# Kernel optimization log

Hardware: AMD Instinct MI355X
Metric: run time of the kernel (lower is better)

Reference implementation:

```python
import jax, jax.numpy as jnp
import numpy as np

N, F, C, H, E, NC = 100000, 128, 64, 4, 1600000, 2
BN_EPS = 1e-5


def _bn(x, g, b):
    mu = x.mean(0)
    var = x.var(0)  # biased variance, as torch BN uses for normalization
    return (x - mu) / jnp.sqrt(var + BN_EPS) * g + b


def _gat(x, src, dst, W, a_src, a_dst, bias, heads, out_ch, concat, n):
    # x:[n,in] -> h:[n,heads,out_ch]
    h = (x @ W).reshape(n, heads, out_ch)
    e_src = (h * a_src[None]).sum(-1)  # [n,heads]
    e_dst = (h * a_dst[None]).sum(-1)
    logits = jax.nn.leaky_relu(e_src[src] + e_dst[dst], 0.2)  # [e,heads]
    m = jax.ops.segment_max(logits, dst, num_segments=n)
    m = jnp.where(jnp.isfinite(m), m, 0.0)
    ex = jnp.exp(logits - m[dst])
    denom = jax.ops.segment_sum(ex, dst, num_segments=n)
    alpha = ex / denom[dst]  # segment softmax over incoming edges
    out = jax.ops.segment_sum(alpha[:, :, None] * h[src], dst, num_segments=n)
    out = out.reshape(n, heads * out_ch) if concat else out.mean(axis=1)
    return out + bias


def _sage(x, src, dst, Wl, bl, Wr, n):
    agg = jax.ops.segment_sum(x[src], dst, num_segments=n)
    cnt = jax.ops.segment_sum(jnp.ones_like(src, dtype=x.dtype), dst, num_segments=n)
    agg = agg / jnp.maximum(cnt, 1.0)[:, None]  # mean aggregation
    return agg @ Wl + bl + x @ Wr


def setup_inputs() -> dict:
    key = jax.random.key(0)
    ks = jax.random.split(key, 24)
    def rn(k, shape, fan):
        return jax.random.normal(k, shape, jnp.float32) * (1.0 / np.sqrt(fan))
    inp = {}
    inp['x'] = jax.random.normal(ks[0], (N, F), jnp.float32)
    inp['edge_index'] = jax.random.randint(ks[1], (2, E), 0, N, jnp.int32)
    # GAT layer 1: in=F, out=C, heads=H, concat
    inp['W1g'] = rn(ks[2], (F, H * C), F)
    inp['a_src1'] = rn(ks[3], (H, C), C)
    inp['a_dst1'] = rn(ks[4], (H, C), C)
    inp['b1g'] = jnp.zeros((H * C,), jnp.float32)
    inp['bn1g_g'] = jnp.ones((H * C,), jnp.float32)
    inp['bn1g_b'] = jnp.zeros((H * C,), jnp.float32)
    # GAT layer 2: in=H*C, out=C, heads=1, no concat
    inp['W2g'] = rn(ks[5], (H * C, C), H * C)
    inp['a_src2'] = rn(ks[6], (1, C), C)
    inp['a_dst2'] = rn(ks[7], (1, C), C)
    inp['b2g'] = jnp.zeros((C,), jnp.float32)
    # SAGE layer 1
    inp['Wl1'] = rn(ks[8], (F, C), F)
    inp['bl1'] = jnp.zeros((C,), jnp.float32)
    inp['Wr1'] = rn(ks[9], (F, C), F)
    inp['bn1s_g'] = jnp.ones((C,), jnp.float32)
    inp['bn1s_b'] = jnp.zeros((C,), jnp.float32)
    # SAGE layer 2
    inp['Wl2'] = rn(ks[10], (C, C), C)
    inp['bl2'] = jnp.zeros((C,), jnp.float32)
    inp['Wr2'] = rn(ks[11], (C, C), C)
    # fusion MLP
    inp['Wf1'] = rn(ks[12], (2 * C, C), 2 * C)
    inp['bf1'] = jnp.zeros((C,), jnp.float32)
    inp['Wf2'] = rn(ks[13], (C, NC), C)
    inp['bf2'] = jnp.zeros((NC,), jnp.float32)
    return inp


def reference(x, edge_index, W1g, a_src1, a_dst1, b1g, bn1g_g, bn1g_b,
              W2g, a_src2, a_dst2, b2g, Wl1, bl1, Wr1, bn1s_g, bn1s_b,
              Wl2, bl2, Wr2, Wf1, bf1, Wf2, bf2):
    n = x.shape[0]
    src, dst = edge_index[0], edge_index[1]
    # PyG GATConv adds self-loops by default
    loop = jnp.arange(n, dtype=src.dtype)
    src_l = jnp.concatenate([src, loop])
    dst_l = jnp.concatenate([dst, loop])

    # GAT branch (dropout = identity in eval)
    g = _gat(x, src_l, dst_l, W1g, a_src1, a_dst1, b1g, H, C, True, n)
    g = jax.nn.elu(_bn(g, bn1g_g, bn1g_b))
    g = _gat(g, src_l, dst_l, W2g, a_src2, a_dst2, b2g, 1, C, False, n)

    # SAGE branch (no self-loops in SAGEConv)
    s = _sage(x, src, dst, Wl1, bl1, Wr1, n)
    s = jax.nn.relu(_bn(s, bn1s_g, bn1s_b))
    s = _sage(s, src, dst, Wl2, bl2, Wr2, n)

    h = jnp.concatenate([g, s], axis=-1)  # [n, 2C]
    h = jax.nn.relu(h @ Wf1 + bf1)
    return h @ Wf2 + bf2  # logits [n, NC]
```

## Files before the change

kernel.cpp:

```cpp
#include <hip/hip_runtime.h>
#include <math.h>


typedef unsigned short u16;
typedef u16 us4 __attribute__((ext_vector_type(4)));
typedef short s8v __attribute__((ext_vector_type(8)));
typedef float f4v __attribute__((ext_vector_type(4)));

__device__ __forceinline__ float b2f(u16 u) {
  union { unsigned int i; float f; } v; v.i = ((unsigned int)u) << 16; return v.f;
}
__device__ __forceinline__ u16 f2b(float f) {
  union { float f; unsigned int i; } v; v.f = f;
  unsigned int u = v.i;
  return (u16)((u + 0x7fffu + ((u >> 16) & 1u)) >> 16);
}

__global__ __launch_bounds__(256) void k_cast(const float* __restrict__ s, u16* __restrict__ d, int n4) {
  int i = blockIdx.x * blockDim.x + threadIdx.x;
  if (i < n4) {
    float4 v = *(reinterpret_cast<const float4*>(s) + i);
    us4 o = { f2b(v.x), f2b(v.y), f2b(v.z), f2b(v.w) };
    *(reinterpret_cast<us4*>(d) + i) = o;
  }
}

struct WcastDesc { const float* W; u16* Wt; int K; int M; };
struct WcastAll { WcastDesc d[5]; };
__global__ __launch_bounds__(256) void k_wcast_all(WcastAll a) {
  WcastDesc de = a.d[blockIdx.y];
  int n = de.K * de.M;
  int idx = blockIdx.x * blockDim.x + threadIdx.x;
  if (idx >= n) return;
  int c = idx / de.K, k = idx - c * de.K;
  de.Wt[idx] = f2b(de.W[(size_t)k * de.M + c]);
}

__global__ __launch_bounds__(256) void k_combine(const float* __restrict__ Wl2, const float* __restrict__ Wr2,
                                                 const float* __restrict__ bl2, const float* __restrict__ Wf1,
                                                 const float* __restrict__ bf1, u16* __restrict__ Wc1t,
                                                 u16* __restrict__ Wc2t, float* __restrict__ biasC) {
  int idx = blockIdx.x * 256 + threadIdx.x;
  if (idx >= 4096) return;
  int m = idx >> 6, k = idx & 63;
  float s1 = 0.f, s2 = 0.f;
  for (int j = 0; j < 64; ++j) {
    float wf = Wf1[(size_t)(64 + j) * 64 + m];
    s1 += Wl2[k * 64 + j] * wf;
    s2 += Wr2[k * 64 + j] * wf;
  }
  Wc1t[m * 64 + k] = f2b(s1);
  Wc2t[m * 64 + k] = f2b(s2);
  if (k == 0) {
    float b = bf1[m];
    for (int j = 0; j < 64; ++j) b += bl2[j] * Wf1[(size_t)(64 + j) * 64 + m];
    biasC[m] = b;
  }
}

__global__ __launch_bounds__(256) void k_deg(const int* __restrict__ ei, int* __restrict__ deg, int E) {
  int e = blockIdx.x * blockDim.x + threadIdx.x;
  if (e < E) atomicAdd(&deg[ei[E + e]], 1);
}

__global__ __launch_bounds__(256) void k_scan1(const int* __restrict__ deg, int* __restrict__ row_ptr,
                                               int* __restrict__ bsum, int n) {
  __shared__ int sh[256];
  int tid = threadIdx.x;
  int i = blockIdx.x * 256 + tid;
  int v = (i < n) ? deg[i] : 0;
  sh[tid] = v;
  __syncthreads();
  for (int off = 1; off < 256; off <<= 1) {
    int t = (tid >= off) ? sh[tid - off] : 0;
    __syncthreads();
    sh[tid] += t;
    __syncthreads();
  }
  if (i < n) row_ptr[i] = sh[tid] - v;
  if (tid == 255) bsum[blockIdx.x] = sh[255];
}

__global__ __launch_bounds__(1024) void k_scan2(int* __restrict__ bsum, int* __restrict__ total, int nb) {
  __shared__ int sh[1024];
  int tid = threadIdx.x;
  int v = (tid < nb) ? bsum[tid] : 0;
  sh[tid] = v;
  __syncthreads();
  for (int off = 1; off < 1024; off <<= 1) {
    int t = (tid >= off) ? sh[tid - off] : 0;
    __syncthreads();
    sh[tid] += t;
    __syncthreads();
  }
  if (tid < nb) bsum[tid] = sh[tid] - v;
  if (tid == 1023) *total = sh[1023];
}

__global__ __launch_bounds__(256) void k_scan3(int* __restrict__ row_ptr, const int* __restrict__ bsum, int n) {
  int i = blockIdx.x * 256 + threadIdx.x;
  if (i < n) row_ptr[i] += bsum[blockIdx.x];
}

__global__ __launch_bounds__(256) void k_scatter(const int* __restrict__ ei, const int* __restrict__ row_ptr,
                                                 int* __restrict__ cursor, int* __restrict__ csr_src, int E) {
  int e = blockIdx.x * blockDim.x + threadIdx.x;
  if (e < E) {
    int d = ei[E + e];
    int pos = row_ptr[d] + atomicAdd(&cursor[d], 1);
    csr_src[pos] = ei[e];
  }
}

struct GemmSeg { const u16* Wt; u16* out; int ldout; const float* bias; };
struct Segs6 { GemmSeg s[6]; };
__global__ __launch_bounds__(256) void k_gemm_multi(const u16* __restrict__ A, int K, Segs6 sg, int Nrows) {
  GemmSeg seg = sg.s[blockIdx.y];
  __shared__ u16 As[64][40];
  __shared__ u16 Bs[64][40];
  int row0 = blockIdx.x * 64;
  int tid = threadIdx.x;
  int w = tid >> 6, lane = tid & 63;
  int lr = tid >> 2;
  int lseg = (tid & 3) * 8;
  f4v acc[4];
#pragma unroll
  for (int n = 0; n < 4; ++n) acc[n] = (f4v){0.f, 0.f, 0.f, 0.f};
  int ar = (w << 4) + (lane & 15);
  int ak = (lane >> 4) << 3;

  for (int k0 = 0; k0 < K; k0 += 32) {
    __syncthreads();
    int gr = row0 + lr;
    s8v av = {};
    if (gr < Nrows) av = *reinterpret_cast<const s8v*>(A + (size_t)gr * K + k0 + lseg);
    *reinterpret_cast<s8v*>(&As[lr][lseg]) = av;
    s8v bv = *reinterpret_cast<const s8v*>(seg.Wt + (size_t)lr * K + k0 + lseg);
    *reinterpret_cast<s8v*>(&Bs[lr][lseg]) = bv;
    __syncthreads();
    s8v af = *reinterpret_cast<const s8v*>(&As[ar][ak]);
#pragma unroll
    for (int n = 0; n < 4; ++n) {
      s8v bf = *reinterpret_cast<const s8v*>(&Bs[(n << 4) + (lane & 15)][ak]);
      acc[n] = __builtin_amdgcn_mfma_f32_16x16x32_bf16(af, bf, acc[n], 0, 0, 0);
    }
  }
  int r0 = row0 + (w << 4) + ((lane >> 4) << 2);
  int cc = lane & 15;
#pragma unroll
  for (int n = 0; n < 4; ++n) {
    int gc = (n << 4) + cc;
    float bv = seg.bias ? seg.bias[gc] : 0.f;
#pragma unroll
    for (int j = 0; j < 4; ++j) {
      int gr = r0 + j;
      if (gr < Nrows) seg.out[(size_t)gr * seg.ldout + gc] = f2b(acc[n][j] + bv);
    }
  }
}

__global__ __launch_bounds__(256) void k_gemm_bn(const u16* __restrict__ A, int K, const u16* __restrict__ Wt,
                                                 const float* __restrict__ sc, const float* __restrict__ sh,
                                                 u16* __restrict__ C, int Nrows, int M) {
  __shared__ u16 As[64][40];
  __shared__ u16 Bs[64][40];
  int row0 = blockIdx.x * 64;
  int tid = threadIdx.x;
  int w = tid >> 6, lane = tid & 63;
  int lr = tid >> 2;
  int lseg = (tid & 3) * 8;
  f4v acc[4];
#pragma unroll
  for (int n = 0; n < 4; ++n) acc[n] = (f4v){0.f, 0.f, 0.f, 0.f};
  int ar = (w << 4) + (lane & 15);
  int ak = (lane >> 4) << 3;

  for (int k0 = 0; k0 < K; k0 += 32) {
    __syncthreads();
    int gr = row0 + lr;
    s8v av = {};
    if (gr < Nrows) {
      av = *reinterpret_cast<const s8v*>(A + (size_t)gr * K + k0 + lseg);
#pragma unroll
      for (int j = 0; j < 8; ++j) {
        int c = k0 + lseg + j;
        float a = b2f((u16)av[j]) * sc[c] + sh[c];
        a = (a > 0.f) ? a : (__expf(a) - 1.f);
        av[j] = (short)f2b(a);
      }
    }
    *reinterpret_cast<s8v*>(&As[lr][lseg]) = av;
    s8v bv = *reinterpret_cast<const s8v*>(Wt + (size_t)lr * K + k0 + lseg);
    *reinterpret_cast<s8v*>(&Bs[lr][lseg]) = bv;
    __syncthreads();
    s8v af = *reinterpret_cast<const s8v*>(&As[ar][ak]);
#pragma unroll
    for (int n = 0; n < 4; ++n) {
      s8v bf = *reinterpret_cast<const s8v*>(&Bs[(n << 4) + (lane & 15)][ak]);
      acc[n] = __builtin_amdgcn_mfma_f32_16x16x32_bf16(af, bf, acc[n], 0, 0, 0);
    }
  }
  int r0 = row0 + (w << 4) + ((lane >> 4) << 2);
  int cc = lane & 15;
#pragma unroll
  for (int n = 0; n < 4; ++n) {
    int gc = (n << 4) + cc;
#pragma unroll
    for (int j = 0; j < 4; ++j) {
      int gr = r0 + j;
      if (gr < Nrows) C[(size_t)gr * M + gc] = f2b(acc[n][j]);
    }
  }
}

__global__ __launch_bounds__(256) void k_gemm_final(const u16* __restrict__ A1, const u16* __restrict__ W1,
                                                    const u16* __restrict__ A2, const u16* __restrict__ W2,
                                                    const u16* __restrict__ A3, const u16* __restrict__ W3,
                                                    const float* __restrict__ biasC, const float* __restrict__ Wf2,
                                                    const float* __restrict__ bf2, float* __restrict__ out,
                                                    int Nrows) {
  __shared__ u16 As[64][40];
  __shared__ u16 Bs[64][40];
  int row0 = blockIdx.x * 64;
  int tid = threadIdx.x;
  int w = tid >> 6, lane = tid & 63;
  int lr = tid >> 2;
  int lseg = (tid & 3) * 8;
  f4v acc[4];
#pragma unroll
  for (int n = 0; n < 4; ++n) acc[n] = (f4v){0.f, 0.f, 0.f, 0.f};
  int ar = (w << 4) + (lane & 15);
  int ak = (lane >> 4) << 3;

  const u16* Aarr[3] = {A1, A2, A3};
  const u16* Warr[3] = {W1, W2, W3};
#pragma unroll
  for (int ph = 0; ph < 3; ++ph) {
    const u16* A = Aarr[ph];
    const u16* Wt = Warr[ph];
#pragma unroll
    for (int k0 = 0; k0 < 64; k0 += 32) {
      __syncthreads();
      int gr = row0 + lr;
      s8v av = {};
      if (gr < Nrows) av = *reinterpret_cast<const s8v*>(A + (size_t)gr * 64 + k0 + lseg);
      *reinterpret_cast<s8v*>(&As[lr][lseg]) = av;
      s8v bv = *reinterpret_cast<const s8v*>(Wt + (size_t)lr * 64 + k0 + lseg);
      *reinterpret_cast<s8v*>(&Bs[lr][lseg]) = bv;
      __syncthreads();
      s8v af = *reinterpret_cast<const s8v*>(&As[ar][ak]);
#pragma unroll
      for (int n = 0; n < 4; ++n) {
        s8v bf = *reinterpret_cast<const s8v*>(&Bs[(n << 4) + (lane & 15)][ak]);
        acc[n] = __builtin_amdgcn_mfma_f32_16x16x32_bf16(af, bf, acc[n], 0, 0, 0);
      }
    }
  }

  int r0 = row0 + (w << 4) + ((lane >> 4) << 2);
  int cc = lane & 15;
  float p0[4] = {0.f, 0.f, 0.f, 0.f}, p1[4] = {0.f, 0.f, 0.f, 0.f};
#pragma unroll
  for (int n = 0; n < 4; ++n) {
    int col = (n << 4) + cc;
    float bC = biasC[col];
    float w0 = Wf2[col * 2 + 0], w1 = Wf2[col * 2 + 1];
#pragma unroll
    for (int j = 0; j < 4; ++j) {
      float f = fmaxf(acc[n][j] + bC, 0.f);
      p0[j] += f * w0;
      p1[j] += f * w1;
    }
  }
#pragma unroll
  for (int off = 1; off < 16; off <<= 1) {
#pragma unroll
    for (int j = 0; j < 4; ++j) {
      p0[j] += __shfl_xor(p0[j], off, 64);
      p1[j] += __shfl_xor(p1[j], off, 64);
    }
  }
  if (cc == 0) {
    float b0 = bf2[0], b1 = bf2[1];
#pragma unroll
    for (int j = 0; j < 4; ++j) {
      int gr = r0 + j;
      if (gr < Nrows) {
        out[(size_t)gr * 2 + 0] = p0[j] + b0;
        out[(size_t)gr * 2 + 1] = p1[j] + b1;
      }
    }
  }
}

template <int H, int C>
__global__ __launch_bounds__(256) void k_attn_prep(const u16* __restrict__ h, const float* __restrict__ a_src,
                                                   const float* __restrict__ a_dst, float* __restrict__ e_src,
                                                   float* __restrict__ e_dst, int n) {
  constexpr int HC = H * C;
  constexpr int VW = HC / 64;
  constexpr int GROUP = C / VW;
  int wid = (blockIdx.x * blockDim.x + threadIdx.x) >> 6;
  int lane = threadIdx.x & 63;
  if (wid >= n) return;
  int c0 = lane * VW;
  float ps = 0.f, pd = 0.f;
  if constexpr (VW == 4) {
    us4 v = *reinterpret_cast<const us4*>(h + (size_t)wid * HC + c0);
#pragma unroll
    for (int j = 0; j < 4; ++j) {
      float hv = b2f(v[j]);
      ps += hv * a_src[c0 + j];
      pd += hv * a_dst[c0 + j];
    }
  } else {
    float hv = b2f(h[(size_t)wid * HC + c0]);
    ps = hv * a_src[c0];
    pd = hv * a_dst[c0];
  }
#pragma unroll
  for (int off = 1; off < GROUP; off <<= 1) {
    ps += __shfl_xor(ps, off, 64);
    pd += __shfl_xor(pd, off, 64);
  }
  if ((lane & (GROUP - 1)) == 0) {
    int hh = c0 / C;
    e_src[(size_t)wid * H + hh] = ps;
    e_dst[(size_t)wid * H + hh] = pd;
  }
}

__global__ __launch_bounds__(256) void k_gat_stats4(const float* __restrict__ es, const float* __restrict__ ed,
                                                    const int* __restrict__ row_ptr, const int* __restrict__ csr,
                                                    float* __restrict__ alphaE, float* __restrict__ alphaS, int n) {
  int wid = (blockIdx.x * blockDim.x + threadIdx.x) >> 6;
  int lane = threadIdx.x & 63;
  if (wid >= n) return;
  int start = row_ptr[wid];
  int deg = row_ptr[wid + 1] - start;
  int h = lane & 3, esl = lane >> 2;
  float edst = ed[(size_t)wid * 4 + h];

  float m = -1e30f, s = 0.f;
  for (int e = esl; e < deg + 1; e += 16) {
    int sn = (e < deg) ? csr[start + e] : wid;
    float v = es[(size_t)sn * 4 + h] + edst;
    v = (v >= 0.f) ? v : 0.2f * v;
    if (v > m) {
      s = s * __expf(m - v) + 1.f;
      m = v;
    } else {
      s += __expf(v - m);
    }
  }
#pragma unroll
  for (int off = 4; off < 64; off <<= 1) {
    float mo = __shfl_xor(m, off, 64);
    float so = __shfl_xor(s, off, 64);
    float M = fmaxf(m, mo);
    s = s * __expf(m - M) + so * __expf(mo - M);
    m = M;
  }
  float invS = 1.f / s;
  for (int e = esl; e < deg + 1; e += 16) {
    int sn = (e < deg) ? csr[start + e] : wid;
    float v = es[(size_t)sn * 4 + h] + edst;
    v = (v >= 0.f) ? v : 0.2f * v;
    float a = __expf(v - m) * invS;
    if (e < deg) alphaE[(size_t)(start + e) * 4 + h] = a;
    else alphaS[(size_t)wid * 4 + h] = a;
  }
}

__global__ __launch_bounds__(256) void k_gat_stats1(const float* __restrict__ es, const float* __restrict__ ed,
                                                    const int* __restrict__ row_ptr, const int* __restrict__ csr,
                                                    float* __restrict__ alphaE, float* __restrict__ alphaS, int n) {
  int wid = (blockIdx.x * blockDim.x + threadIdx.x) >> 6;
  int lane = threadIdx.x & 63;
  if (wid >= n) return;
  int start = row_ptr[wid];
  int deg = row_ptr[wid + 1] - start;
  float edst = ed[wid];
  float m = -1e30f, s = 0.f;
  for (int e = lane; e < deg + 1; e += 64) {
    int sn = (e < deg) ? csr[start + e] : wid;
    float v = es[sn] + edst;
    v = (v >= 0.f) ? v : 0.2f * v;
    if (v > m) {
      s = s * __expf(m - v) + 1.f;
      m = v;
    } else {
      s += __expf(v - m);
    }
  }
#pragma unroll
  for (int off = 1; off < 64; off <<= 1) {
    float mo = __shfl_xor(m, off, 64);
    float so = __shfl_xor(s, off, 64);
    float M = fmaxf(m, mo);
    s = s * __expf(m - M) + so * __expf(mo - M);
    m = M;
  }
  float invS = 1.f / s;
  for (int e = lane; e < deg + 1; e += 64) {
    int sn = (e < deg) ? csr[start + e] : wid;
    float v = es[sn] + edst;
    v = (v >= 0.f) ? v : 0.2f * v;
    float a = __expf(v - m) * invS;
    if (e < deg) alphaE[start + e] = a;
    else alphaS[wid] = a;
  }
}

template <int H, int C>
__global__ __launch_bounds__(256) void k_gat_agg2(const u16* __restrict__ h, const float* __restrict__ alphaE,
                                                  const float* __restrict__ alphaS, const int* __restrict__ row_ptr,
                                                  const int* __restrict__ csr, const float* __restrict__ bias,
                                                  u16* __restrict__ out, int n) {
  constexpr int HC = H * C;
  constexpr int VW = HC / 64;
  int wid = (blockIdx.x * blockDim.x + threadIdx.x) >> 6;
  int lane = threadIdx.x & 63;
  if (wid >= n) return;
  int start = row_ptr[wid];
  int deg = row_ptr[wid + 1] - start;
  int hl = (lane * VW) / C;

  float acc[VW];
  {
    float aS = alphaS[(size_t)wid * H + hl];
    if constexpr (VW == 4) {
      us4 hv = *(reinterpret_cast<const us4*>(h + (size_t)wid * HC) + lane);
#pragma unroll
      for (int j = 0; j < 4; ++j) acc[j] = aS * b2f(hv[j]);
    } else {
      acc[0] = aS * b2f(h[(size_t)wid * HC + lane]);
    }
  }

  int e = 0;
  for (; e + 4 <= deg; e += 4) {
    int sn[4];
    float al[4];
#pragma unroll
    for (int i = 0; i < 4; ++i) {
      sn[i] = csr[start + e + i];
      al[i] = alphaE[(size_t)(start + e + i) * H + hl];
    }
#pragma unroll
    for (int i = 0; i < 4; ++i) {
      if constexpr (VW == 4) {
        us4 hv = *(reinterpret_cast<const us4*>(h + (size_t)sn[i] * HC) + lane);
#pragma unroll
        for (int j = 0; j < 4; ++j) acc[j] += al[i] * b2f(hv[j]);
      } else {
        acc[0] += al[i] * b2f(h[(size_t)sn[i] * HC + lane]);
      }
    }
  }
  for (; e < deg; ++e) {
    int sn = csr[start + e];
    float al = alphaE[(size_t)(start + e) * H + hl];
    if constexpr (VW == 4) {
      us4 hv = *(reinterpret_cast<const us4*>(h + (size_t)sn * HC) + lane);
#pragma unroll
      for (int j = 0; j < 4; ++j) acc[j] += al * b2f(hv[j]);
    } else {
      acc[0] += al * b2f(h[(size_t)sn * HC + lane]);
    }
  }

  int c0 = lane * VW;
#pragma unroll
  for (int j = 0; j < VW; ++j) out[(size_t)wid * HC + c0 + j] = f2b(acc[j] + bias[c0 + j]);
}

__global__ __launch_bounds__(256) void k_sage_agg64(const u16* __restrict__ x, const int* __restrict__ row_ptr,
                                                    const int* __restrict__ csr, const u16* __restrict__ Cin,
                                                    u16* __restrict__ agg, int n) {
  int wid = (blockIdx.x * blockDim.x + threadIdx.x) >> 6;
  int lane = threadIdx.x & 63;
  if (wid >= n) return;
  int start = row_ptr[wid];
  int deg = row_ptr[wid + 1] - start;
  float acc = 0.f;
  int e = 0;
  for (; e + 4 <= deg; e += 4) {
    int sn[4];
#pragma unroll
    for (int i = 0; i < 4; ++i) sn[i] = csr[start + e + i];
#pragma unroll
    for (int i = 0; i < 4; ++i) acc += b2f(x[(size_t)sn[i] * 64 + lane]);
  }
  for (; e < deg; ++e) acc += b2f(x[(size_t)csr[start + e] * 64 + lane]);
  float inv = 1.f / fmaxf((float)deg, 1.f);
  float base = Cin ? b2f(Cin[(size_t)wid * 64 + lane]) : 0.f;
  agg[(size_t)wid * 64 + lane] = f2b(acc * inv + base);
}

template <int CH>
__global__ __launch_bounds__(256) void k_bn_stats(const u16* __restrict__ x, float* __restrict__ stats, int n) {
  constexpr int RPB = 256 / CH;
  int tid = threadIdx.x;
  int c = tid % CH;
  int rsub = tid / CH;
  float s = 0.f, q = 0.f;
  for (int r = blockIdx.x * RPB + rsub; r < n; r += gridDim.x * RPB) {
    float v = b2f(x[(size_t)r * CH + c]);
    s += v;
    q += v * v;
  }
  __shared__ float ls[256], lq[256];
  ls[tid] = s; lq[tid] = q;
  __syncthreads();
  if (tid < CH) {
#pragma unroll
    for (int i = 1; i < RPB; ++i) { s += ls[tid + i * CH]; q += lq[tid + i * CH]; }
    atomicAdd(&stats[c], s);
    atomicAdd(&stats[CH + c], q);
  }
}

template <int CH>
__global__ __launch_bounds__(256) void k_bn_final(const float* __restrict__ stats, const float* __restrict__ gamma,
                                                  const float* __restrict__ beta, float* __restrict__ sc,
                                                  float* __restrict__ sh, int n) {
  int c = threadIdx.x;
  if (c >= CH) return;
  float invn = 1.f / (float)n;
  float mu = stats[c] * invn;
  float var = stats[CH + c] * invn - mu * mu;
  float rs = rsqrtf(var + 1e-5f);
  sc[c] = rs * gamma[c];
  sh[c] = beta[c] - mu * rs * gamma[c];
}

template <int CH>
__global__ __launch_bounds__(256) void k_bn_apply(u16* __restrict__ x, const float* __restrict__ stats,
                                                  const float* __restrict__ gamma, const float* __restrict__ beta,
                                                  int n, int act) {
  float invn = 1.f / (float)n;
  size_t total = (size_t)n * CH;
  for (size_t idx = (size_t)blockIdx.x * blockDim.x + threadIdx.x; idx < total;
       idx += (size_t)gridDim.x * blockDim.x) {
    int c = (int)(idx % CH);
    float mu = stats[c] * invn;
    float var = stats[CH + c] * invn - mu * mu;
    float v = (b2f(x[idx]) - mu) * rsqrtf(var + 1e-5f) * gamma[c] + beta[c];
    if (act == 1) v = fmaxf(v, 0.f);
    else v = (v > 0.f) ? v : (__expf(v) - 1.f);
    x[idx] = f2b(v);
  }
}

extern "C" void kernel_launch(void* const* d_in, const int* in_sizes, int n_in,
                              void* d_out, int out_size, void* d_ws, size_t ws_size,
                              hipStream_t stream) {
  const float* x      = (const float*)d_in[0];
  const int*   ei     = (const int*)d_in[1];
  const float* W1g    = (const float*)d_in[2];
  const float* a_src1 = (const float*)d_in[3];
  const float* a_dst1 = (const float*)d_in[4];
  const float* b1g    = (const float*)d_in[5];
  const float* bn1g_g = (const float*)d_in[6];
  const float* bn1g_b = (const float*)d_in[7];
  const float* W2g    = (const float*)d_in[8];
  const float* a_src2 = (const float*)d_in[9];
  const float* a_dst2 = (const float*)d_in[10];
  const float* b2g    = (const float*)d_in[11];
  const float* Wl1    = (const float*)d_in[12];
  const float* bl1    = (const float*)d_in[13];
  const float* Wr1    = (const float*)d_in[14];
  const float* bn1s_g = (const float*)d_in[15];
  const float* bn1s_b = (const float*)d_in[16];
  const float* Wl2    = (const float*)d_in[17];
  const float* bl2    = (const float*)d_in[18];
  const float* Wr2    = (const float*)d_in[19];
  const float* Wf1    = (const float*)d_in[20];
  const float* bf1    = (const float*)d_in[21];
  const float* Wf2    = (const float*)d_in[22];
  const float* bf2    = (const float*)d_in[23];

  const int N = in_sizes[0] / 128;
  const int E = in_sizes[1] / 2;

  char* ws = (char*)d_ws;
  size_t off = 0;
  auto alloc = [&](size_t bytes) -> void* {
    size_t o = (off + 255) & ~(size_t)255;
    off = o + bytes;
    return (void*)(ws + o);
  };

  u16* xb    = (u16*)alloc((size_t)N * 128 * 2);
  u16* h1b   = (u16*)alloc((size_t)N * 256 * 2);
  u16* gb    = (u16*)alloc((size_t)N * 256 * 2);
  u16* h2b   = (u16*)alloc((size_t)N * 64 * 2);
  u16* g2b   = (u16*)alloc((size_t)N * 64 * 2);
  u16* xlb   = (u16*)alloc((size_t)N * 64 * 2);
  u16* xrb   = (u16*)alloc((size_t)N * 64 * 2);
  u16* s1b   = (u16*)alloc((size_t)N * 64 * 2);
  float* es1 = (float*)alloc((size_t)N * 4 * 4);
  float* ed1 = (float*)alloc((size_t)N * 4 * 4);
  float* es2 = (float*)alloc((size_t)N * 4);
  float* ed2 = (float*)alloc((size_t)N * 4);
  float* alphaE = (float*)alloc((size_t)E * 4 * 4);
  float* alphaS = (float*)alloc((size_t)N * 4 * 4);
  int* deg     = (int*)alloc((size_t)N * 2 * 4);
  int* cursor  = deg + N;
  int* row_ptr = (int*)alloc((size_t)(N + 1) * 4);
  int* bsum    = (int*)alloc(1024 * 4);
  int* csr     = (int*)alloc((size_t)E * 4);
  float* statsG = (float*)alloc((512 + 128) * 4);
  float* statsS = statsG + 512;
  float* scg   = (float*)alloc(256 * 4);
  float* shg   = (float*)alloc(256 * 4);
  float* biasC = (float*)alloc(64 * 4);
  u16* W1t  = (u16*)alloc(256 * 128 * 2);
  u16* W2t  = (u16*)alloc(64 * 256 * 2);
  u16* Wl1t = (u16*)alloc(64 * 128 * 2);
  u16* Wr1t = (u16*)alloc(64 * 128 * 2);
  u16* Wf1at= (u16*)alloc(64 * 64 * 2);
  u16* Wc1t = (u16*)alloc(64 * 64 * 2);
  u16* Wc2t = (u16*)alloc(64 * 64 * 2);
  u16* sagg2b = h1b;

  const int tb = 256;
  const int nwb = (N + 3) / 4;
  const int nsb = (N + 255) / 256;

  hipMemsetAsync(deg, 0, (size_t)N * 2 * 4, stream);
  hipMemsetAsync(statsG, 0, (512 + 128) * 4, stream);
  k_deg<<<(E + tb - 1) / tb, tb, 0, stream>>>(ei, deg, E);
  k_scan1<<<nsb, 256, 0, stream>>>(deg, row_ptr, bsum, N);
  k_scan2<<<1, 1024, 0, stream>>>(bsum, row_ptr + N, nsb);
  k_scan3<<<nsb, 256, 0, stream>>>(row_ptr, bsum, N);
  k_scatter<<<(E + tb - 1) / tb, tb, 0, stream>>>(ei, row_ptr, cursor, csr, E);

  k_cast<<<((N * 128 / 4) + tb - 1) / tb, tb, 0, stream>>>(x, xb, N * 128 / 4);
  WcastAll wa;
  wa.d[0] = { W1g, W1t, 128, 256 };
  wa.d[1] = { W2g, W2t, 256, 64 };
  wa.d[2] = { Wl1, Wl1t, 128, 64 };
  wa.d[3] = { Wr1, Wr1t, 128, 64 };
  wa.d[4] = { Wf1, Wf1at, 64, 64 };
  dim3 wgrid((128 * 256 + tb - 1) / tb, 5);
  k_wcast_all<<<wgrid, tb, 0, stream>>>(wa);
  k_combine<<<16, 256, 0, stream>>>(Wl2, Wr2, bl2, Wf1, bf1, Wc1t, Wc2t, biasC);

  const int gx = (N + 63) / 64;

  Segs6 sg;
  sg.s[0] = { W1t,            h1b,       256, nullptr };
  sg.s[1] = { W1t + 64 * 128, h1b + 64,  256, nullptr };
  sg.s[2] = { W1t + 128 * 128, h1b + 128, 256, nullptr };
  sg.s[3] = { W1t + 192 * 128, h1b + 192, 256, nullptr };
  sg.s[4] = { Wl1t,           xlb,       64,  nullptr };
  sg.s[5] = { Wr1t,           xrb,       64,  bl1 };
  k_gemm_multi<<<dim3(gx, 6), 256, 0, stream>>>(xb, 128, sg, N);

  k_attn_prep<4, 64><<<nwb, 256, 0, stream>>>(h1b, a_src1, a_dst1, es1, ed1, N);
  k_gat_stats4<<<nwb, 256, 0, stream>>>(es1, ed1, row_ptr, csr, alphaE, alphaS, N);
  k_gat_agg2<4, 64><<<nwb, 256, 0, stream>>>(h1b, alphaE, alphaS, row_ptr, csr, b1g, gb, N);
  k_bn_stats<256><<<256, 256, 0, stream>>>(gb, statsG, N);
  k_bn_final<256><<<1, 256, 0, stream>>>(statsG, bn1g_g, bn1g_b, scg, shg, N);

  k_sage_agg64<<<nwb, 256, 0, stream>>>(xlb, row_ptr, csr, xrb, s1b, N);
  k_bn_stats<64><<<256, 256, 0, stream>>>(s1b, statsS, N);
  k_bn_apply<64><<<2048, 256, 0, stream>>>(s1b, statsS, bn1s_g, bn1s_b, N, 1);

  k_gemm_bn<<<dim3(gx, 1), 256, 0, stream>>>(gb, 256, W2t, scg, shg, h2b, N, 64);
  k_attn_prep<1, 64><<<nwb, 256, 0, stream>>>(h2b, a_src2, a_dst2, es2, ed2, N);
  k_gat_stats1<<<nwb, 256, 0, stream>>>(es2, ed2, row_ptr, csr, alphaE, alphaS, N);
  k_gat_agg2<1, 64><<<nwb, 256, 0, stream>>>(h2b, alphaE, alphaS, row_ptr, csr, b2g, g2b, N);

  k_sage_agg64<<<nwb, 256, 0, stream>>>(s1b, row_ptr, csr, nullptr, sagg2b, N);

  k_gemm_final<<<dim3(gx, 1), 256, 0, stream>>>(g2b, Wf1at, sagg2b, Wc1t, s1b, Wc2t,
                                                biasC, Wf2, bf2, (float*)d_out, N);
}
```

Baseline: 825.5 us.

## Fuse GAT softmax into aggregation and fold casts, attention prep, BN apply into GEMMs

Several kernels are merged. The x-to-bf16 cast goes into the first GEMM, which now computes all six weight segments from one A tile and also produces the attention logits. The per-edge alpha materialisation (alphaE and alphaS) is replaced by a per-node online softmax held in LDS, with recompute for nodes of degree above 256. The SAGE BatchNorm apply is folded into the second aggregation and the final GEMM. The aim is to cut large intermediate global-memory traffic (E×4 alpha floats, the xb copy, the BN rewrite) and several launches, at the cost of heavier registers and LDS in the fused GEMM and extra exp work.

```diff
diff --git a/kernel.cpp b/kernel.cpp
--- a/kernel.cpp
+++ b/kernel.cpp
@@ -14,15 +14,6 @@
   union { float f; unsigned int i; } v; v.f = f;
   unsigned int u = v.i;
   return (u16)((u + 0x7fffu + ((u >> 16) & 1u)) >> 16);
-}
-
-__global__ __launch_bounds__(256) void k_cast(const float* __restrict__ s, u16* __restrict__ d, int n4) {
-  int i = blockIdx.x * blockDim.x + threadIdx.x;
-  if (i < n4) {
-    float4 v = *(reinterpret_cast<const float4*>(s) + i);
-    us4 o = { f2b(v.x), f2b(v.y), f2b(v.z), f2b(v.w) };
-    *(reinterpret_cast<us4*>(d) + i) = o;
-  }
 }
 
 struct WcastDesc { const float* W; u16* Wt; int K; int M; };
@@ -112,10 +103,113 @@
   }
 }
 
-struct GemmSeg { const u16* Wt; u16* out; int ldout; const float* bias; };
-struct Segs6 { GemmSeg s[6]; };
-__global__ __launch_bounds__(256) void k_gemm_multi(const u16* __restrict__ A, int K, Segs6 sg, int Nrows) {
-  GemmSeg seg = sg.s[blockIdx.y];
+struct Seg6Ptr { const u16* Wt[6]; };
+__global__ __launch_bounds__(256) void k_gemm_fused1(const float* __restrict__ X, Seg6Ptr wp,
+                                                     u16* __restrict__ h1, u16* __restrict__ xl,
+                                                     u16* __restrict__ xr, const float* __restrict__ bl1,
+                                                     const float* __restrict__ a_src1, const float* __restrict__ a_dst1,
+                                                     float* __restrict__ es1, float* __restrict__ ed1, int Nrows) {
+  __shared__ u16 As[64][40];
+  __shared__ u16 Bs[6][64][40];
+  int row0 = blockIdx.x * 64;
+  int tid = threadIdx.x;
+  int w = tid >> 6, lane = tid & 63;
+  int lr = tid >> 2;
+  int lseg = (tid & 3) * 8;
+  f4v acc[6][4];
+#pragma unroll
+  for (int s = 0; s < 6; ++s)
+#pragma unroll
+    for (int nn = 0; nn < 4; ++nn) acc[s][nn] = (f4v){0.f, 0.f, 0.f, 0.f};
+  int ar = (w << 4) + (lane & 15);
+  int ak = (lane >> 4) << 3;
+
+  for (int k0 = 0; k0 < 128; k0 += 32) {
+    __syncthreads();
+    int gr = row0 + lr;
+    s8v av = {};
+    if (gr < Nrows) {
+      float4 lo = *reinterpret_cast<const float4*>(X + (size_t)gr * 128 + k0 + lseg);
+      float4 hi = *reinterpret_cast<const float4*>(X + (size_t)gr * 128 + k0 + lseg + 4);
+      av[0] = (short)f2b(lo.x); av[1] = (short)f2b(lo.y); av[2] = (short)f2b(lo.z); av[3] = (short)f2b(lo.w);
+      av[4] = (short)f2b(hi.x); av[5] = (short)f2b(hi.y); av[6] = (short)f2b(hi.z); av[7] = (short)f2b(hi.w);
+    }
+    *reinterpret_cast<s8v*>(&As[lr][lseg]) = av;
+#pragma unroll
+    for (int s = 0; s < 6; ++s) {
+      s8v bv = *reinterpret_cast<const s8v*>(wp.Wt[s] + (size_t)lr * 128 + k0 + lseg);
+      *reinterpret_cast<s8v*>(&Bs[s][lr][lseg]) = bv;
+    }
+    __syncthreads();
+    s8v af = *reinterpret_cast<const s8v*>(&As[ar][ak]);
+#pragma unroll
+    for (int s = 0; s < 6; ++s) {
+#pragma unroll
+      for (int nn = 0; nn < 4; ++nn) {
+        s8v bf = *reinterpret_cast<const s8v*>(&Bs[s][(nn << 4) + (lane & 15)][ak]);
+        acc[s][nn] = __builtin_amdgcn_mfma_f32_16x16x32_bf16(af, bf, acc[s][nn], 0, 0, 0);
+      }
+    }
+  }
+
+  int r0 = row0 + (w << 4) + ((lane >> 4) << 2);
+  int cc = lane & 15;
+#pragma unroll
+  for (int s = 0; s < 4; ++s) {
+    float pe[4] = {0.f, 0.f, 0.f, 0.f}, pd[4] = {0.f, 0.f, 0.f, 0.f};
+#pragma unroll
+    for (int nn = 0; nn < 4; ++nn) {
+      int col = (nn << 4) + cc;
+      float asv = a_src1[s * 64 + col];
+      float adv = a_dst1[s * 64 + col];
+#pragma unroll
+      for (int j = 0; j < 4; ++j) {
+        float hv = acc[s][nn][j];
+        pe[j] += hv * asv;
+        pd[j] += hv * adv;
+        int gr = r0 + j;
+        if (gr < Nrows) h1[(size_t)gr * 256 + s * 64 + col] = f2b(hv);
+      }
+    }
+#pragma unroll
+    for (int off = 1; off < 16; off <<= 1) {
+#pragma unroll
+      for (int j = 0; j < 4; ++j) {
+        pe[j] += __shfl_xor(pe[j], off, 64);
+        pd[j] += __shfl_xor(pd[j], off, 64);
+      }
+    }
+    if (cc == 0) {
+#pragma unroll
+      for (int j = 0; j < 4; ++j) {
+        int gr = r0 + j;
+        if (gr < Nrows) {
+          es1[(size_t)gr * 4 + s] = pe[j];
+          ed1[(size_t)gr * 4 + s] = pd[j];
+        }
+      }
+    }
+  }
+#pragma unroll
+  for (int nn = 0; nn < 4; ++nn) {
+    int gc = (nn << 4) + cc;
+    float bv = bl1[gc];
+#pragma unroll
+    for (int j = 0; j < 4; ++j) {
+      int gr = r0 + j;
+      if (gr < Nrows) {
+        xl[(size_t)gr * 64 + gc] = f2b(acc[4][nn][j]);
+        xr[(size_t)gr * 64 + gc] = f2b(acc[5][nn][j] + bv);
+      }
+    }
+  }
+}
+
+__global__ __launch_bounds__(256) void k_gemm_bn(const u16* __restrict__ A, const u16* __restrict__ Wt,
+                                                 const float* __restrict__ sc, const float* __restrict__ sh,
+                                                 const float* __restrict__ a_src2, const float* __restrict__ a_dst2,
+                                                 u16* __restrict__ C, float* __restrict__ es2,
+                                                 float* __restrict__ ed2, int Nrows) {
   __shared__ u16 As[64][40];
   __shared__ u16 Bs[64][40];
   int row0 = blockIdx.x * 64;
@@ -125,62 +219,16 @@
   int lseg = (tid & 3) * 8;
   f4v acc[4];
 #pragma unroll
-  for (int n = 0; n < 4; ++n) acc[n] = (f4v){0.f, 0.f, 0.f, 0.f};
+  for (int nn = 0; nn < 4; ++nn) acc[nn] = (f4v){0.f, 0.f, 0.f, 0.f};
   int ar = (w << 4) + (lane & 15);
   int ak = (lane >> 4) << 3;
 
-  for (int k0 = 0; k0 < K; k0 += 32) {
-    __syncthreads();
-    int gr = row0 + lr;
-    s8v av = {};
-    if (gr < Nrows) av = *reinterpret_cast<const s8v*>(A + (size_t)gr * K + k0 + lseg);
-    *reinterpret_cast<s8v*>(&As[lr][lseg]) = av;
-    s8v bv = *reinterpret_cast<const s8v*>(seg.Wt + (size_t)lr * K + k0 + lseg);
-    *reinterpret_cast<s8v*>(&Bs[lr][lseg]) = bv;
-    __syncthreads();
-    s8v af = *reinterpret_cast<const s8v*>(&As[ar][ak]);
-#pragma unroll
-    for (int n = 0; n < 4; ++n) {
-      s8v bf = *reinterpret_cast<const s8v*>(&Bs[(n << 4) + (lane & 15)][ak]);
-      acc[n] = __builtin_amdgcn_mfma_f32_16x16x32_bf16(af, bf, acc[n], 0, 0, 0);
-    }
-  }
-  int r0 = row0 + (w << 4) + ((lane >> 4) << 2);
-  int cc = lane & 15;
-#pragma unroll
-  for (int n = 0; n < 4; ++n) {
-    int gc = (n << 4) + cc;
-    float bv = seg.bias ? seg.bias[gc] : 0.f;
-#pragma unroll
-    for (int j = 0; j < 4; ++j) {
-      int gr = r0 + j;
-      if (gr < Nrows) seg.out[(size_t)gr * seg.ldout + gc] = f2b(acc[n][j] + bv);
-    }
-  }
-}
-
-__global__ __launch_bounds__(256) void k_gemm_bn(const u16* __restrict__ A, int K, const u16* __restrict__ Wt,
-                                                 const float* __restrict__ sc, const float* __restrict__ sh,
-                                                 u16* __restrict__ C, int Nrows, int M) {
-  __shared__ u16 As[64][40];
-  __shared__ u16 Bs[64][40];
-  int row0 = blockIdx.x * 64;
-  int tid = threadIdx.x;
-  int w = tid >> 6, lane = tid & 63;
-  int lr = tid >> 2;
-  int lseg = (tid & 3) * 8;
-  f4v acc[4];
-#pragma unroll
-  for (int n = 0; n < 4; ++n) acc[n] = (f4v){0.f, 0.f, 0.f, 0.f};
-  int ar = (w << 4) + (lane & 15);
-  int ak = (lane >> 4) << 3;
-
-  for (int k0 = 0; k0 < K; k0 += 32) {
+  for (int k0 = 0; k0 < 256; k0 += 32) {
     __syncthreads();
     int gr = row0 + lr;
     s8v av = {};
     if (gr < Nrows) {
-      av = *reinterpret_cast<const s8v*>(A + (size_t)gr * K + k0 + lseg);
+      av = *reinterpret_cast<const s8v*>(A + (size_t)gr * 256 + k0 + lseg);
 #pragma unroll
       for (int j = 0; j < 8; ++j) {
         int c = k0 + lseg + j;
@@ -190,32 +238,253 @@
       }
     }
     *reinterpret_cast<s8v*>(&As[lr][lseg]) = av;
-    s8v bv = *reinterpret_cast<const s8v*>(Wt + (size_t)lr * K + k0 + lseg);
+    s8v bv = *reinterpret_cast<const s8v*>(Wt + (size_t)lr * 256 + k0 + lseg);
     *reinterpret_cast<s8v*>(&Bs[lr][lseg]) = bv;
     __syncthreads();
     s8v af = *reinterpret_cast<const s8v*>(&As[ar][ak]);
 #pragma unroll
-    for (int n = 0; n < 4; ++n) {
-      s8v bf = *reinterpret_cast<const s8v*>(&Bs[(n << 4) + (lane & 15)][ak]);
-      acc[n] = __builtin_amdgcn_mfma_f32_16x16x32_bf16(af, bf, acc[n], 0, 0, 0);
+    for (int nn = 0; nn < 4; ++nn) {
+      s8v bf = *reinterpret_cast<const s8v*>(&Bs[(nn << 4) + (lane & 15)][ak]);
+      acc[nn] = __builtin_amdgcn_mfma_f32_16x16x32_bf16(af, bf, acc[nn], 0, 0, 0);
     }
   }
   int r0 = row0 + (w << 4) + ((lane >> 4) << 2);
   int cc = lane & 15;
-#pragma unroll
-  for (int n = 0; n < 4; ++n) {
-    int gc = (n << 4) + cc;
+  float pe[4] = {0.f, 0.f, 0.f, 0.f}, pd[4] = {0.f, 0.f, 0.f, 0.f};
+#pragma unroll
+  for (int nn = 0; nn < 4; ++nn) {
+    int gc = (nn << 4) + cc;
+    float asv = a_src2[gc], adv = a_dst2[gc];
+#pragma unroll
+    for (int j = 0; j < 4; ++j) {
+      float hv = acc[nn][j];
+      pe[j] += hv * asv;
+      pd[j] += hv * adv;
+      int gr = r0 + j;
+      if (gr < Nrows) C[(size_t)gr * 64 + gc] = f2b(hv);
+    }
+  }
+#pragma unroll
+  for (int off = 1; off < 16; off <<= 1) {
+#pragma unroll
+    for (int j = 0; j < 4; ++j) {
+      pe[j] += __shfl_xor(pe[j], off, 64);
+      pd[j] += __shfl_xor(pd[j], off, 64);
+    }
+  }
+  if (cc == 0) {
 #pragma unroll
     for (int j = 0; j < 4; ++j) {
       int gr = r0 + j;
-      if (gr < Nrows) C[(size_t)gr * M + gc] = f2b(acc[n][j]);
-    }
+      if (gr < Nrows) { es2[gr] = pe[j]; ed2[gr] = pd[j]; }
+    }
+  }
+}
+
+template <int H>
+__global__ __launch_bounds__(256) void k_gat_fused(const u16* __restrict__ h, const float* __restrict__ es,
+                                                   const float* __restrict__ ed, const int* __restrict__ row_ptr,
+                                                   const int* __restrict__ csr, const float* __restrict__ bias,
+                                                   u16* __restrict__ out, int n) {
+  constexpr int HC = H * 64;
+  constexpr int VW = HC / 64;
+  constexpr int SL = 64 / H;
+  constexpr int CAP = 256;
+  __shared__ float lal[4][CAP * H];
+  int widx = threadIdx.x >> 6;
+  int wid = blockIdx.x * 4 + widx;
+  int lane = threadIdx.x & 63;
+  float* A = lal[widx];
+  bool active = wid < n;
+  int start = 0, deg = 0;
+  if (active) { start = row_ptr[wid]; deg = row_ptr[wid + 1] - start; }
+  int ne = deg + 1;
+
+  int hh = lane % H;
+  int esl = lane / H;
+  float m = -1e30f, s = 0.f;
+  if (active) {
+    float edst = ed[(size_t)wid * H + hh];
+    for (int e = esl; e < ne; e += SL) {
+      int sn = (e < deg) ? csr[start + e] : wid;
+      float v = es[(size_t)sn * H + hh] + edst;
+      v = (v >= 0.f) ? v : 0.2f * v;
+      if (e < CAP) A[e * H + hh] = v;
+      if (v > m) { s = s * __expf(m - v) + 1.f; m = v; }
+      else s += __expf(v - m);
+    }
+  }
+#pragma unroll
+  for (int off = H; off < 64; off <<= 1) {
+    float mo = __shfl_xor(m, off, 64);
+    float so = __shfl_xor(s, off, 64);
+    float M = fmaxf(m, mo);
+    s = s * __expf(m - M) + so * __expf(mo - M);
+    m = M;
+  }
+  float invS = 1.f / s;
+  if (active) {
+    int lim = (ne < CAP) ? ne : CAP;
+    for (int e = esl; e < lim; e += SL) A[e * H + hh] = __expf(A[e * H + hh] - m) * invS;
+  }
+  __syncthreads();
+
+  if (active) {
+    int c0 = lane * VW;
+    int hl = c0 >> 6;
+    float mh = __shfl(m, hl, 64);
+    float iSh = __shfl(invS, hl, 64);
+    float edl = 0.f;
+    if (ne > CAP) edl = ed[(size_t)wid * H + hl];
+    float acc[VW] = {};
+    {
+      float aS;
+      if (deg < CAP) aS = A[deg * H + hl];
+      else {
+        float v = es[(size_t)wid * H + hl] + edl;
+        v = (v >= 0.f) ? v : 0.2f * v;
+        aS = __expf(v - mh) * iSh;
+      }
+      if constexpr (VW == 4) {
+        us4 hv = *(reinterpret_cast<const us4*>(h + (size_t)wid * HC) + lane);
+#pragma unroll
+        for (int j = 0; j < 4; ++j) acc[j] = aS * b2f(hv[j]);
+      } else {
+        acc[0] = aS * b2f(h[(size_t)wid * HC + lane]);
+      }
+    }
+    int e = 0;
+    for (; e + 4 <= deg; e += 4) {
+      int sn[4];
+      float al[4];
+#pragma unroll
+      for (int i = 0; i < 4; ++i) {
+        sn[i] = csr[start + e + i];
+        if (e + i < CAP) al[i] = A[(e + i) * H + hl];
+        else {
+          float v = es[(size_t)sn[i] * H + hl] + edl;
+          v = (v >= 0.f) ? v : 0.2f * v;
+          al[i] = __expf(v - mh) * iSh;
+        }
+      }
+#pragma unroll
+      for (int i = 0; i < 4; ++i) {
+        if constexpr (VW == 4) {
+          us4 hv = *(reinterpret_cast<const us4*>(h + (size_t)sn[i] * HC) + lane);
+#pragma unroll
+          for (int j = 0; j < 4; ++j) acc[j] += al[i] * b2f(hv[j]);
+        } else {
+          acc[0] += al[i] * b2f(h[(size_t)sn[i] * HC + lane]);
+        }
+      }
+    }
+    for (; e < deg; ++e) {
+      int sn = csr[start + e];
+      float al;
+      if (e < CAP) al = A[e * H + hl];
+      else {
+        float v = es[(size_t)sn * H + hl] + edl;
+        v = (v >= 0.f) ? v : 0.2f * v;
+        al = __expf(v - mh) * iSh;
+      }
+      if constexpr (VW == 4) {
+        us4 hv = *(reinterpret_cast<const us4*>(h + (size_t)sn * HC) + lane);
+#pragma unroll
+        for (int j = 0; j < 4; ++j) acc[j] += al * b2f(hv[j]);
+      } else {
+        acc[0] += al * b2f(h[(size_t)sn * HC + lane]);
+      }
+    }
+#pragma unroll
+    for (int j = 0; j < VW; ++j) out[(size_t)wid * HC + c0 + j] = f2b(acc[j] + bias[c0 + j]);
+  }
+}
+
+__global__ __launch_bounds__(256) void k_sage_agg64(const u16* __restrict__ x, const int* __restrict__ row_ptr,
+                                                    const int* __restrict__ csr, const u16* __restrict__ Cin,
+                                                    const float* __restrict__ sc, const float* __restrict__ sh,
+                                                    u16* __restrict__ agg, int n) {
+  int wid = (blockIdx.x * blockDim.x + threadIdx.x) >> 6;
+  int lane = threadIdx.x & 63;
+  if (wid >= n) return;
+  int start = row_ptr[wid];
+  int deg = row_ptr[wid + 1] - start;
+  bool bn = sc != nullptr;
+  float scv = 1.f, shv = 0.f;
+  if (bn) { scv = sc[lane]; shv = sh[lane]; }
+  float acc = 0.f;
+  int e = 0;
+  for (; e + 4 <= deg; e += 4) {
+    int sn[4];
+#pragma unroll
+    for (int i = 0; i < 4; ++i) sn[i] = csr[start + e + i];
+#pragma unroll
+    for (int i = 0; i < 4; ++i) {
+      float v = b2f(x[(size_t)sn[i] * 64 + lane]);
+      if (bn) v = fmaxf(v * scv + shv, 0.f);
+      acc += v;
+    }
+  }
+  for (; e < deg; ++e) {
+    float v = b2f(x[(size_t)csr[start + e] * 64 + lane]);
+    if (bn) v = fmaxf(v * scv + shv, 0.f);
+    acc += v;
+  }
+  float inv = 1.f / fmaxf((float)deg, 1.f);
+  float base = Cin ? b2f(Cin[(size_t)wid * 64 + lane]) : 0.f;
+  agg[(size_t)wid * 64 + lane] = f2b(acc * inv + base);
+}
+
+template <int CH>
+__global__ __launch_bounds__(256) void k_bn_stats(const u16* __restrict__ x, float* __restrict__ stats, int n) {
+  constexpr int RPB = 256 / CH;
+  int tid = threadIdx.x;
+  int c = tid % CH;
+  int rsub = tid / CH;
+  float s = 0.f, q = 0.f;
+  for (int r = blockIdx.x * RPB + rsub; r < n; r += gridDim.x * RPB) {
+    float v = b2f(x[(size_t)r * CH + c]);
+    s += v;
+    q += v * v;
+  }
+  __shared__ float ls[256], lq[256];
+  ls[tid] = s; lq[tid] = q;
+  __syncthreads();
+  if (tid < CH) {
+#pragma unroll
+    for (int i = 1; i < RPB; ++i) { s += ls[tid + i * CH]; q += lq[tid + i * CH]; }
+    atomicAdd(&stats[c], s);
+    atomicAdd(&stats[CH + c], q);
+  }
+}
+
+__global__ __launch_bounds__(256) void k_bn_final2(const float* __restrict__ statsG, const float* __restrict__ statsS,
+                                                   const float* __restrict__ gG, const float* __restrict__ bG,
+                                                   const float* __restrict__ gS, const float* __restrict__ bS,
+                                                   float* __restrict__ scG, float* __restrict__ shG,
+                                                   float* __restrict__ scS, float* __restrict__ shS, int n) {
+  int c = threadIdx.x;
+  float invn = 1.f / (float)n;
+  {
+    float mu = statsG[c] * invn;
+    float var = statsG[256 + c] * invn - mu * mu;
+    float rs = rsqrtf(var + 1e-5f) * gG[c];
+    scG[c] = rs;
+    shG[c] = bG[c] - mu * rs;
+  }
+  if (c < 64) {
+    float mu = statsS[c] * invn;
+    float var = statsS[64 + c] * invn - mu * mu;
+    float rs = rsqrtf(var + 1e-5f) * gS[c];
+    scS[c] = rs;
+    shS[c] = bS[c] - mu * rs;
   }
 }
 
 __global__ __launch_bounds__(256) void k_gemm_final(const u16* __restrict__ A1, const u16* __restrict__ W1,
                                                     const u16* __restrict__ A2, const u16* __restrict__ W2,
                                                     const u16* __restrict__ A3, const u16* __restrict__ W3,
+                                                    const float* __restrict__ scS, const float* __restrict__ shS,
                                                     const float* __restrict__ biasC, const float* __restrict__ Wf2,
                                                     const float* __restrict__ bf2, float* __restrict__ out,
                                                     int Nrows) {
@@ -228,7 +497,7 @@
   int lseg = (tid & 3) * 8;
   f4v acc[4];
 #pragma unroll
-  for (int n = 0; n < 4; ++n) acc[n] = (f4v){0.f, 0.f, 0.f, 0.f};
+  for (int nn = 0; nn < 4; ++nn) acc[nn] = (f4v){0.f, 0.f, 0.f, 0.f};
   int ar = (w << 4) + (lane & 15);
   int ak = (lane >> 4) << 3;
 
@@ -243,16 +512,26 @@
       __syncthreads();
       int gr = row0 + lr;
       s8v av = {};
-      if (gr < Nrows) av = *reinterpret_cast<const s8v*>(A + (size_t)gr * 64 + k0 + lseg);
+      if (gr < Nrows) {
+        av = *reinterpret_cast<const s8v*>(A + (size_t)gr * 64 + k0 + lseg);
+        if (ph == 2) {
+#pragma unroll
+          for (int j = 0; j < 8; ++j) {
+            int c = k0 + lseg + j;
+            float a = fmaxf(b2f((u16)av[j]) * scS[c] + shS[c], 0.f);
+            av[j] = (short)f2b(a);
+          }
+        }
+      }
       *reinterpret_cast<s8v*>(&As[lr][lseg]) = av;
       s8v bv = *reinterpret_cast<const s8v*>(Wt + (size_t)lr * 64 + k0 + lseg);
       *reinterpret_cast<s8v*>(&Bs[lr][lseg]) = bv;
       __syncthreads();
       s8v af = *reinterpret_cast<const s8v*>(&As[ar][ak]);
 #pragma unroll
-      for (int n = 0; n < 4; ++n) {
-        s8v bf = *reinterpret_cast<const s8v*>(&Bs[(n << 4) + (lane & 15)][ak]);
-        acc[n] = __builtin_amdgcn_mfma_f32_16x16x32_bf16(af, bf, acc[n], 0, 0, 0);
+      for (int nn = 0; nn < 4; ++nn) {
+        s8v bf = *reinterpret_cast<const s8v*>(&Bs[(nn << 4) + (lane & 15)][ak]);
+        acc[nn] = __builtin_amdgcn_mfma_f32_16x16x32_bf16(af, bf, acc[nn], 0, 0, 0);
       }
     }
   }
@@ -261,13 +540,13 @@
   int cc = lane & 15;
   float p0[4] = {0.f, 0.f, 0.f, 0.f}, p1[4] = {0.f, 0.f, 0.f, 0.f};
 #pragma unroll
-  for (int n = 0; n < 4; ++n) {
-    int col = (n << 4) + cc;
+  for (int nn = 0; nn < 4; ++nn) {
+    int col = (nn << 4) + cc;
     float bC = biasC[col];
     float w0 = Wf2[col * 2 + 0], w1 = Wf2[col * 2 + 1];
 #pragma unroll
     for (int j = 0; j < 4; ++j) {
-      float f = fmaxf(acc[n][j] + bC, 0.f);
+      float f = fmaxf(acc[nn][j] + bC, 0.f);
       p0[j] += f * w0;
       p1[j] += f * w1;
     }
@@ -290,266 +569,6 @@
         out[(size_t)gr * 2 + 1] = p1[j] + b1;
       }
     }
-  }
-}
-
-template <int H, int C>
-__global__ __launch_bounds__(256) void k_attn_prep(const u16* __restrict__ h, const float* __restrict__ a_src,
-                                                   const float* __restrict__ a_dst, float* __restrict__ e_src,
-                                                   float* __restrict__ e_dst, int n) {
-  constexpr int HC = H * C;
-  constexpr int VW = HC / 64;
-  constexpr int GROUP = C / VW;
-  int wid = (blockIdx.x * blockDim.x + threadIdx.x) >> 6;
-  int lane = threadIdx.x & 63;
-  if (wid >= n) return;
-  int c0 = lane * VW;
-  float ps = 0.f, pd = 0.f;
-  if constexpr (VW == 4) {
-    us4 v = *reinterpret_cast<const us4*>(h + (size_t)wid * HC + c0);
-#pragma unroll
-    for (int j = 0; j < 4; ++j) {
-      float hv = b2f(v[j]);
-      ps += hv * a_src[c0 + j];
-      pd += hv * a_dst[c0 + j];
-    }
-  } else {
-    float hv = b2f(h[(size_t)wid * HC + c0]);
-    ps = hv * a_src[c0];
-    pd = hv * a_dst[c0];
-  }
-#pragma unroll
-  for (int off = 1; off < GROUP; off <<= 1) {
-    ps += __shfl_xor(ps, off, 64);
-    pd += __shfl_xor(pd, off, 64);
-  }
-  if ((lane & (GROUP - 1)) == 0) {
-    int hh = c0 / C;
-    e_src[(size_t)wid * H + hh] = ps;
-    e_dst[(size_t)wid * H + hh] = pd;
-  }
-}
-
-__global__ __launch_bounds__(256) void k_gat_stats4(const float* __restrict__ es, const float* __restrict__ ed,
-                                                    const int* __restrict__ row_ptr, const int* __restrict__ csr,
-                                                    float* __restrict__ alphaE, float* __restrict__ alphaS, int n) {
-  int wid = (blockIdx.x * blockDim.x + threadIdx.x) >> 6;
-  int lane = threadIdx.x & 63;
-  if (wid >= n) return;
-  int start = row_ptr[wid];
-  int deg = row_ptr[wid + 1] - start;
-  int h = lane & 3, esl = lane >> 2;
-  float edst = ed[(size_t)wid * 4 + h];
-
-  float m = -1e30f, s = 0.f;
-  for (int e = esl; e < deg + 1; e += 16) {
-    int sn = (e < deg) ? csr[start + e] : wid;
-    float v = es[(size_t)sn * 4 + h] + edst;
-    v = (v >= 0.f) ? v : 0.2f * v;
-    if (v > m) {
-      s = s * __expf(m - v) + 1.f;
-      m = v;
-    } else {
-      s += __expf(v - m);
-    }
-  }
-#pragma unroll
-  for (int off = 4; off < 64; off <<= 1) {
-    float mo = __shfl_xor(m, off, 64);
-    float so = __shfl_xor(s, off, 64);
-    float M = fmaxf(m, mo);
-    s = s * __expf(m - M) + so * __expf(mo - M);
-    m = M;
-  }
-  float invS = 1.f / s;
-  for (int e = esl; e < deg + 1; e += 16) {
-    int sn = (e < deg) ? csr[start + e] : wid;
-    float v = es[(size_t)sn * 4 + h] + edst;
-    v = (v >= 0.f) ? v : 0.2f * v;
-    float a = __expf(v - m) * invS;
-    if (e < deg) alphaE[(size_t)(start + e) * 4 + h] = a;
-    else alphaS[(size_t)wid * 4 + h] = a;
-  }
-}
-
-__global__ __launch_bounds__(256) void k_gat_stats1(const float* __restrict__ es, const float* __restrict__ ed,
-                                                    const int* __restrict__ row_ptr, const int* __restrict__ csr,
-                                                    float* __restrict__ alphaE, float* __restrict__ alphaS, int n) {
-  int wid = (blockIdx.x * blockDim.x + threadIdx.x) >> 6;
-  int lane = threadIdx.x & 63;
-  if (wid >= n) return;
-  int start = row_ptr[wid];
-  int deg = row_ptr[wid + 1] - start;
-  float edst = ed[wid];
-  float m = -1e30f, s = 0.f;
-  for (int e = lane; e < deg + 1; e += 64) {
-    int sn = (e < deg) ? csr[start + e] : wid;
-    float v = es[sn] + edst;
-    v = (v >= 0.f) ? v : 0.2f * v;
-    if (v > m) {
-      s = s * __expf(m - v) + 1.f;
-      m = v;
-    } else {
-      s += __expf(v - m);
-    }
-  }
-#pragma unroll
-  for (int off = 1; off < 64; off <<= 1) {
-    float mo = __shfl_xor(m, off, 64);
-    float so = __shfl_xor(s, off, 64);
-    float M = fmaxf(m, mo);
-    s = s * __expf(m - M) + so * __expf(mo - M);
-    m = M;
-  }
-  float invS = 1.f / s;
-  for (int e = lane; e < deg + 1; e += 64) {
-    int sn = (e < deg) ? csr[start + e] : wid;
-    float v = es[sn] + edst;
-    v = (v >= 0.f) ? v : 0.2f * v;
-    float a = __expf(v - m) * invS;
-    if (e < deg) alphaE[start + e] = a;
-    else alphaS[wid] = a;
-  }
-}
-
-template <int H, int C>
-__global__ __launch_bounds__(256) void k_gat_agg2(const u16* __restrict__ h, const float* __restrict__ alphaE,
-                                                  const float* __restrict__ alphaS, const int* __restrict__ row_ptr,
-                                                  const int* __restrict__ csr, const float* __restrict__ bias,
-                                                  u16* __restrict__ out, int n) {
-  constexpr int HC = H * C;
-  constexpr int VW = HC / 64;
-  int wid = (blockIdx.x * blockDim.x + threadIdx.x) >> 6;
-  int lane = threadIdx.x & 63;
-  if (wid >= n) return;
-  int start = row_ptr[wid];
-  int deg = row_ptr[wid + 1] - start;
-  int hl = (lane * VW) / C;
-
-  float acc[VW];
-  {
-    float aS = alphaS[(size_t)wid * H + hl];
-    if constexpr (VW == 4) {
-      us4 hv = *(reinterpret_cast<const us4*>(h + (size_t)wid * HC) + lane);
-#pragma unroll
-      for (int j = 0; j < 4; ++j) acc[j] = aS * b2f(hv[j]);
-    } else {
-      acc[0] = aS * b2f(h[(size_t)wid * HC + lane]);
-    }
-  }
-
-  int e = 0;
-  for (; e + 4 <= deg; e += 4) {
-    int sn[4];
-    float al[4];
-#pragma unroll
-    for (int i = 0; i < 4; ++i) {
-      sn[i] = csr[start + e + i];
-      al[i] = alphaE[(size_t)(start + e + i) * H + hl];
-    }
-#pragma unroll
-    for (int i = 0; i < 4; ++i) {
-      if constexpr (VW == 4) {
-        us4 hv = *(reinterpret_cast<const us4*>(h + (size_t)sn[i] * HC) + lane);
-#pragma unroll
-        for (int j = 0; j < 4; ++j) acc[j] += al[i] * b2f(hv[j]);
-      } else {
-        acc[0] += al[i] * b2f(h[(size_t)sn[i] * HC + lane]);
-      }
-    }
-  }
-  for (; e < deg; ++e) {
-    int sn = csr[start + e];
-    float al = alphaE[(size_t)(start + e) * H + hl];
-    if constexpr (VW == 4) {
-      us4 hv = *(reinterpret_cast<const us4*>(h + (size_t)sn * HC) + lane);
-#pragma unroll
-      for (int j = 0; j < 4; ++j) acc[j] += al * b2f(hv[j]);
-    } else {
-      acc[0] += al * b2f(h[(size_t)sn * HC + lane]);
-    }
-  }
-
-  int c0 = lane * VW;
-#pragma unroll
-  for (int j = 0; j < VW; ++j) out[(size_t)wid * HC + c0 + j] = f2b(acc[j] + bias[c0 + j]);
-}
-
-__global__ __launch_bounds__(256) void k_sage_agg64(const u16* __restrict__ x, const int* __restrict__ row_ptr,
-                                                    const int* __restrict__ csr, const u16* __restrict__ Cin,
-                                                    u16* __restrict__ agg, int n) {
-  int wid = (blockIdx.x * blockDim.x + threadIdx.x) >> 6;
-  int lane = threadIdx.x & 63;
-  if (wid >= n) return;
-  int start = row_ptr[wid];
-  int deg = row_ptr[wid + 1] - start;
-  float acc = 0.f;
-  int e = 0;
-  for (; e + 4 <= deg; e += 4) {
-    int sn[4];
-#pragma unroll
-    for (int i = 0; i < 4; ++i) sn[i] = csr[start + e + i];
-#pragma unroll
-    for (int i = 0; i < 4; ++i) acc += b2f(x[(size_t)sn[i] * 64 + lane]);
-  }
-  for (; e < deg; ++e) acc += b2f(x[(size_t)csr[start + e] * 64 + lane]);
-  float inv = 1.f / fmaxf((float)deg, 1.f);
-  float base = Cin ? b2f(Cin[(size_t)wid * 64 + lane]) : 0.f;
-  agg[(size_t)wid * 64 + lane] = f2b(acc * inv + base);
-}
-
-template <int CH>
-__global__ __launch_bounds__(256) void k_bn_stats(const u16* __restrict__ x, float* __restrict__ stats, int n) {
-  constexpr int RPB = 256 / CH;
-  int tid = threadIdx.x;
-  int c = tid % CH;
-  int rsub = tid / CH;
-  float s = 0.f, q = 0.f;
-  for (int r = blockIdx.x * RPB + rsub; r < n; r += gridDim.x * RPB) {
-    float v = b2f(x[(size_t)r * CH + c]);
-    s += v;
-    q += v * v;
-  }
-  __shared__ float ls[256], lq[256];
-  ls[tid] = s; lq[tid] = q;
-  __syncthreads();
-  if (tid < CH) {
-#pragma unroll
-    for (int i = 1; i < RPB; ++i) { s += ls[tid + i * CH]; q += lq[tid + i * CH]; }
-    atomicAdd(&stats[c], s);
-    atomicAdd(&stats[CH + c], q);
-  }
-}
-
-template <int CH>
-__global__ __launch_bounds__(256) void k_bn_final(const float* __restrict__ stats, const float* __restrict__ gamma,
-                                                  const float* __restrict__ beta, float* __restrict__ sc,
-                                                  float* __restrict__ sh, int n) {
-  int c = threadIdx.x;
-  if (c >= CH) return;
-  float invn = 1.f / (float)n;
-  float mu = stats[c] * invn;
-  float var = stats[CH + c] * invn - mu * mu;
-  float rs = rsqrtf(var + 1e-5f);
-  sc[c] = rs * gamma[c];
-  sh[c] = beta[c] - mu * rs * gamma[c];
-}
-
-template <int CH>
-__global__ __launch_bounds__(256) void k_bn_apply(u16* __restrict__ x, const float* __restrict__ stats,
-                                                  const float* __restrict__ gamma, const float* __restrict__ beta,
-                                                  int n, int act) {
-  float invn = 1.f / (float)n;
-  size_t total = (size_t)n * CH;
-  for (size_t idx = (size_t)blockIdx.x * blockDim.x + threadIdx.x; idx < total;
-       idx += (size_t)gridDim.x * blockDim.x) {
-    int c = (int)(idx % CH);
-    float mu = stats[c] * invn;
-    float var = stats[CH + c] * invn - mu * mu;
-    float v = (b2f(x[idx]) - mu) * rsqrtf(var + 1e-5f) * gamma[c] + beta[c];
-    if (act == 1) v = fmaxf(v, 0.f);
-    else v = (v > 0.f) ? v : (__expf(v) - 1.f);
-    x[idx] = f2b(v);
   }
 }
 
@@ -592,7 +611,6 @@
     return (void*)(ws + o);
   };
 
-  u16* xb    = (u16*)alloc((size_t)N * 128 * 2);
   u16* h1b   = (u16*)alloc((size_t)N * 256 * 2);
   u16* gb    = (u16*)alloc((size_t)N * 256 * 2);
   u16* h2b   = (u16*)alloc((size_t)N * 64 * 2);
@@ -604,8 +622,6 @@
   float* ed1 = (float*)alloc((size_t)N * 4 * 4);
   float* es2 = (float*)alloc((size_t)N * 4);
   float* ed2 = (float*)alloc((size_t)N * 4);
-  float* alphaE = (float*)alloc((size_t)E * 4 * 4);
-  float* alphaS = (float*)alloc((size_t)N * 4 * 4);
   int* deg     = (int*)alloc((size_t)N * 2 * 4);
   int* cursor  = deg + N;
   int* row_ptr = (int*)alloc((size_t)(N + 1) * 4);
@@ -615,6 +631,8 @@
   float* statsS = statsG + 512;
   float* scg   = (float*)alloc(256 * 4);
   float* shg   = (float*)alloc(256 * 4);
+  float* scs   = (float*)alloc(64 * 4);
+  float* shs   = (float*)alloc(64 * 4);
   float* biasC = (float*)alloc(64 * 4);
   u16* W1t  = (u16*)alloc(256 * 128 * 2);
   u16* W2t  = (u16*)alloc(64 * 256 * 2);
@@ -628,6 +646,7 @@
   const int tb = 256;
   const int nwb = (N + 3) / 4;
   const int nsb = (N + 255) / 256;
+  const int gx = (N + 63) / 64;
 
   hipMemsetAsync(deg, 0, (size_t)N * 2 * 4, stream);
   hipMemsetAsync(statsG, 0, (512 + 128) * 4, stream);
@@ -637,7 +656,6 @@
   k_scan3<<<nsb, 256, 0, stream>>>(row_ptr, bsum, N);
   k_scatter<<<(E + tb - 1) / tb, tb, 0, stream>>>(ei, row_ptr, cursor, csr, E);
 
-  k_cast<<<((N * 128 / 4) + tb - 1) / tb, tb, 0, stream>>>(x, xb, N * 128 / 4);
   WcastAll wa;
   wa.d[0] = { W1g, W1t, 128, 256 };
   wa.d[1] = { W2g, W2t, 256, 64 };
@@ -648,34 +666,28 @@
   k_wcast_all<<<wgrid, tb, 0, stream>>>(wa);
   k_combine<<<16, 256, 0, stream>>>(Wl2, Wr2, bl2, Wf1, bf1, Wc1t, Wc2t, biasC);
 
-  const int gx = (N + 63) / 64;
-
-  Segs6 sg;
-  sg.s[0] = { W1t,            h1b,       256, nullptr };
-  sg.s[1] = { W1t + 64 * 128, h1b + 64,  256, nullptr };
-  sg.s[2] = { W1t + 128 * 128, h1b + 128, 256, nullptr };
-  sg.s[3] = { W1t + 192 * 128, h1b + 192, 256, nullptr };
-  sg.s[4] = { Wl1t,           xlb,       64,  nullptr };
-  sg.s[5] = { Wr1t,           xrb,       64,  bl1 };
-  k_gemm_multi<<<dim3(gx, 6), 256, 0, stream>>>(xb, 128, sg, N);
-
-  k_attn_prep<4, 64><<<nwb, 256, 0, stream>>>(h1b, a_src1, a_dst1, es1, ed1, N);
-  k_gat_stats4<<<nwb, 256, 0, stream>>>(es1, ed1, row_ptr, csr, alphaE, alphaS, N);
-  k_gat_agg2<4, 64><<<nwb, 256, 0, stream>>>(h1b, alphaE, alphaS, row_ptr, csr, b1g, gb, N);
+  Seg6Ptr sp;
+  sp.Wt[0] = W1t;
+  sp.Wt[1] = W1t + 64 * 128;
+  sp.Wt[2] = W1t + 128 * 128;
+  sp.Wt[3] = W1t + 192 * 128;
+  sp.Wt[4] = Wl1t;
+  sp.Wt[5] = Wr1t;
+  k_gemm_fused1<<<gx, 256, 0, stream>>>(x, sp, h1b, xlb, xrb, bl1, a_src1, a_dst1, es1, ed1, N);
+
+  k_gat_fused<4><<<nwb, 256, 0, stream>>>(h1b, es1, ed1, row_ptr, csr, b1g, gb, N);
   k_bn_stats<256><<<256, 256, 0, stream>>>(gb, statsG, N);
-  k_bn_final<256><<<1, 256, 0, stream>>>(statsG, bn1g_g, bn1g_b, scg, shg, N);
-
-  k_sage_agg64<<<nwb, 256, 0, stream>>>(xlb, row_ptr, csr, xrb, s1b, N);
+
+  k_sage_agg64<<<nwb, 256, 0, stream>>>(xlb, row_ptr, csr, xrb, nullptr, nullptr, s1b, N);
   k_bn_stats<64><<<256, 256, 0, stream>>>(s1b, statsS, N);
-  k_bn_apply<64><<<2048, 256, 0, stream>>>(s1b, statsS, bn1s_g, bn1s_b, N, 1);
-
-  k_gemm_bn<<<dim3(gx, 1), 256, 0, stream>>>(gb, 256, W2t, scg, shg, h2b, N, 64);
-  k_attn_prep<1, 64><<<nwb, 256, 0, stream>>>(h2b, a_src2, a_dst2, es2, ed2, N);
-  k_gat_stats1<<<nwb, 256, 0, stream>>>(es2, ed2, row_ptr, csr, alphaE, alphaS, N);
-  k_gat_agg2<1, 64><<<nwb, 256, 0, stream>>>(h2b, alphaE, alphaS, row_ptr, csr, b2g, g2b, N);
-
-  k_sage_agg64<<<nwb, 256, 0, stream>>>(s1b, row_ptr, csr, nullptr, sagg2b, N);
-
-  k_gemm_final<<<dim3(gx, 1), 256, 0, stream>>>(g2b, Wf1at, sagg2b, Wc1t, s1b, Wc2t,
-                                                biasC, Wf2, bf2, (float*)d_out, N);
-}
+  k_bn_final2<<<1, 256, 0, stream>>>(statsG, statsS, bn1g_g, bn1g_b, bn1s_g, bn1s_b,
+                                     scg, shg, scs, shs, N);
+
+  k_gemm_bn<<<gx, 256, 0, stream>>>(gb, W2t, scg, shg, a_src2, a_dst2, h2b, es2, ed2, N);
+  k_gat_fused<1><<<nwb, 256, 0, stream>>>(h2b, es2, ed2, row_ptr, csr, b2g, g2b, N);
+
+  k_sage_agg64<<<nwb, 256, 0, stream>>>(s1b, row_ptr, csr, nullptr, scs, shs, sagg2b, N);
+
+  k_gemm_final<<<gx, 256, 0, stream>>>(g2b, Wf1at, sagg2b, Wc1t, s1b, Wc2t,
+                                       scs, shs, biasC, Wf2, bf2, (float*)d_out, N);
+}
```

Measured after the change: 836.1 us. About the same (+1.3%).
